# Optimization experiments

Hardware: AMD Instinct MI355X
Metric: run time of the kernel (lower is better)

## Reference

```python
import jax, jax.numpy as jnp
import numpy as np
from jax import lax

N, C, H, W = 16, 1, 512, 512
MAX_ITERS = H + W  # upper bound on flood-fill propagation distance


def _dilate4(r):
    # 3x3 cross (4-connectivity) grayscale dilation, r: (N,H,W)
    rp = jnp.pad(r, ((0, 0), (1, 1), (1, 1)))
    up = rp[:, :-2, 1:-1]
    dn = rp[:, 2:, 1:-1]
    lf = rp[:, 1:-1, :-2]
    rt = rp[:, 1:-1, 2:]
    return jnp.maximum(jnp.maximum(jnp.maximum(up, dn), jnp.maximum(lf, rt)), r)


def _reconstruct_dilation(marker, mask):
    # skimage.morphology.reconstruction(seed, mask, method='dilation'):
    # iterate rec = min(dilate(rec), mask) until convergence.
    def cond(state):
        _, changed, i = state
        return jnp.logical_and(changed, i < MAX_ITERS)

    def body(state):
        r, _, i = state
        nr = jnp.minimum(_dilate4(r), mask)
        return nr, jnp.any(nr != r), i + 1

    rec, _, _ = lax.while_loop(cond, body, (marker, jnp.array(True), jnp.array(0)))
    return rec


def _adaptive_binarize(prob, marker_factor, mask_factor):
    # prob: (N,1,H,W); mirrors torch .detach() -> threshold -> reconstruction
    img = lax.stop_gradient(prob[:, 0])  # (N,H,W)
    nzm = img > 0
    cnt = jnp.sum(nzm, axis=(1, 2))                      # (N,)
    safe = jnp.maximum(cnt, 1).astype(img.dtype)
    mean = jnp.sum(jnp.where(nzm, img, 0.0), axis=(1, 2)) / safe
    var = jnp.sum(jnp.where(nzm, (img - mean[:, None, None]) ** 2, 0.0), axis=(1, 2)) / safe
    std = jnp.sqrt(var)

    def threshold(factor):
        T = (mean + factor * std)[:, None, None]
        b = img > T
        empty = jnp.sum(b, axis=(1, 2)) == 0
        T2 = (mean + (factor / 2.0) * std)[:, None, None]
        b2 = img > T2
        return jnp.where(empty[:, None, None], b2, b)

    marker = threshold(marker_factor).astype(jnp.float32)
    maskb = threshold(mask_factor).astype(jnp.float32)
    rec = _reconstruct_dilation(marker, maskb)
    out = (rec > 0.5).astype(jnp.float32)
    out = jnp.where((cnt == 0)[:, None, None], 0.0, out)  # no nonzero pixels -> zeros
    return out[:, None]  # (N,1,H,W)


def setup_inputs() -> dict:
    key = jax.random.key(0)
    k1, k2 = jax.random.split(key)
    thick_logit = jax.random.normal(k1, (N, C, H, W), dtype=jnp.float32)
    thin_logit = jax.random.normal(k2, (N, C, H, W), dtype=jnp.float32)
    return {"thick_logit": thick_logit, "thin_logit": thin_logit}


def reference(thick_logit, thin_logit):
    thick_prob = jax.nn.sigmoid(thick_logit)
    thin_prob = jax.nn.sigmoid(thin_logit)
    thick_bin = _adaptive_binarize(thick_prob, 2.0, 0.5)
    thin_bin = _adaptive_binarize(thin_prob, 4.0, 0.5)
    fused_bin = jnp.clip(thick_bin + thin_bin, 0.0, 1.0)
    return thick_logit, thin_logit, fused_bin
```

## Files before the change

kernel.cpp:

```cpp
#include <hip/hip_runtime.h>
#include <cstdint>
#include <cstddef>

#define HW 512
#define NPIX (HW * HW)
#define NIMG 16
#define NII 32
#define CHUNKS 64
#define CHUNK_PIX 4096
#define IN_ELEMS (NIMG * NPIX)
#define WORDS_PER_II 4096

#define WS_PARTA   0u
#define WS_STATS   49152u
#define WS_PARTC   50176u
#define WS_SEL     82944u
#define WS_ZMASK   83456u
#define WS_MP      98304u
#define WS_MF      (WS_MP + 1048576u)
#define WS_KP      (WS_MF + 1048576u)
#define WS_KF      (WS_KP + 1048576u)
#define WS_ROUT    (WS_KF + 1048576u)

typedef unsigned long long u64;

__device__ __forceinline__ float sigmoid_f32(float x) {
    return (float)(1.0 / (1.0 + exp(-(double)x)));
}

__global__ void kA_copy_reduce(const float* __restrict__ thick,
                               const float* __restrict__ thin,
                               float* __restrict__ out,
                               double* __restrict__ partA) {
    int b = blockIdx.x;
    int ii = b >> 6;
    int chunk = b & 63;
    int j = ii >> 4, n = ii & 15;
    const float* src = (j == 0 ? thick : thin) + (size_t)n * NPIX;
    float* dst = out + (size_t)j * IN_ELEMS + (size_t)n * NPIX;
    int base = chunk * CHUNK_PIX;

    double s = 0.0, sq = 0.0, c = 0.0;
    for (int i = 0; i < 16; ++i) {
        int e = base + i * 256 + threadIdx.x;
        float x = src[e];
        dst[e] = x;
        float img = sigmoid_f32(x);
        if (img > 0.0f) {
            double d = (double)img;
            s += d; sq += d * d; c += 1.0;
        }
    }
    __shared__ double sm[256], sv[256], sc[256];
    sm[threadIdx.x] = s; sv[threadIdx.x] = sq; sc[threadIdx.x] = c;
    __syncthreads();
    for (int off = 128; off > 0; off >>= 1) {
        if (threadIdx.x < off) {
            sm[threadIdx.x] += sm[threadIdx.x + off];
            sv[threadIdx.x] += sv[threadIdx.x + off];
            sc[threadIdx.x] += sc[threadIdx.x + off];
        }
        __syncthreads();
    }
    if (threadIdx.x == 0) {
        double* p = partA + (size_t)(ii * 64 + chunk) * 3;
        p[0] = sm[0]; p[1] = sv[0]; p[2] = sc[0];
    }
}

__global__ void kB_stats(const double* __restrict__ partA,
                         double* __restrict__ stats) {
    int ii = blockIdx.x;
    int t = threadIdx.x;
    const double* p = partA + (size_t)(ii * 64 + t) * 3;
    double s = p[0], sq = p[1], c = p[2];
    for (int off = 32; off > 0; off >>= 1) {
        s  += __shfl_down(s,  (unsigned)off, 64);
        sq += __shfl_down(sq, (unsigned)off, 64);
        c  += __shfl_down(c,  (unsigned)off, 64);
    }
    if (t == 0) {
        double mean = 0.0, var = 0.0;
        if (c > 0.0) {
            mean = s / c;
            var = sq / c - mean * mean;
            if (var < 0.0) var = 0.0;
        }
        double* o = stats + (size_t)ii * 4;
        o[0] = mean; o[1] = sqrt(var); o[2] = c; o[3] = 0.0;
    }
}

__global__ void kC_bitmaps(const float* __restrict__ thick,
                           const float* __restrict__ thin,
                           const double* __restrict__ stats,
                           u64* __restrict__ mp, u64* __restrict__ mf,
                           u64* __restrict__ kp, u64* __restrict__ kf,
                           long long* __restrict__ partC) {
    int b = blockIdx.x;
    int ii = b >> 6;
    int chunk = b & 63;
    int j = ii >> 4, n = ii & 15;
    const float* src = (j == 0 ? thick : thin) + (size_t)n * NPIX;
    const double* st = stats + (size_t)ii * 4;
    double mean = st[0], sd = st[1];
    double fac = (j == 0) ? 2.0 : 4.0;
    double Tm  = mean + fac * sd;
    double Tmh = mean + (fac * 0.5) * sd;
    double Tk  = mean + 0.5 * sd;
    double Tkh = mean + 0.25 * sd;

    int t = threadIdx.x, lane = t & 63, w = t >> 6;
    long long cM = 0, cK = 0;
    for (int i = 0; i < 16; ++i) {
        int e = chunk * CHUNK_PIX + i * 256 + t;
        float x = src[e];
        double img = (double)sigmoid_f32(x);
        u64 bM  = __ballot(img > Tm);
        u64 bMh = __ballot(img > Tmh);
        u64 bK  = __ballot(img > Tk);
        u64 bKh = __ballot(img > Tkh);
        if (lane == 0) {
            size_t g = (size_t)ii * WORDS_PER_II + (size_t)chunk * 64 + i * 4 + w;
            mp[g] = bM; mf[g] = bMh; kp[g] = bK; kf[g] = bKh;
            cM += (long long)__popcll(bM);
            cK += (long long)__popcll(bK);
        }
    }
    __shared__ long long aM[4], aK[4];
    if (lane == 0) { aM[w] = cM; aK[w] = cK; }
    __syncthreads();
    if (t == 0) {
        long long* p = partC + (size_t)(ii * 64 + chunk) * 2;
        p[0] = aM[0] + aM[1] + aM[2] + aM[3];
        p[1] = aK[0] + aK[1] + aK[2] + aK[3];
    }
}

__global__ void kD_select(const long long* __restrict__ partC,
                          const double* __restrict__ stats,
                          int* __restrict__ sel,
                          u64* __restrict__ zmask) {
    int ii = threadIdx.x;
    if (ii < NII) {
        long long cM = 0, cK = 0;
        for (int c = 0; c < 64; ++c) {
            const long long* p = partC + (size_t)(ii * 64 + c) * 2;
            cM += p[0]; cK += p[1];
        }
        sel[ii * 4 + 0] = (cM == 0) ? 1 : 0;
        sel[ii * 4 + 1] = (cK == 0) ? 1 : 0;
        zmask[ii] = (stats[(size_t)ii * 4 + 2] > 0.0) ? ~0ull : 0ull;
    }
}

__global__ __launch_bounds__(512) void kE_flood(const u64* __restrict__ mp,
                                                const u64* __restrict__ mf,
                                                const u64* __restrict__ kp,
                                                const u64* __restrict__ kf,
                                                const int* __restrict__ sel,
                                                u64* __restrict__ rout) {
    int ii = blockIdx.x;
    const u64* M = (sel[ii * 4 + 0] ? mf : mp) + (size_t)ii * WORDS_PER_II;
    const u64* K = (sel[ii * 4 + 1] ? kf : kp) + (size_t)ii * WORDS_PER_II;

    __shared__ u64 R[WORDS_PER_II];
    __shared__ int changed;
    int t = threadIdx.x;

    u64 kreg[8];
    for (int w = 0; w < 8; ++w) {
        kreg[w] = K[(size_t)t * 8 + w];
        R[w * HW + t] = M[(size_t)t * 8 + w];
    }
    if (t == 0) changed = 0;
    __syncthreads();

    for (int it = 0; it < 1024; ++it) {
        u64 cur[8], up[8], dn[8];
        for (int w = 0; w < 8; ++w) {
            cur[w] = R[w * HW + t];
            up[w] = (t > 0)        ? R[w * HW + (t - 1)] : 0ull;
            dn[w] = (t < HW - 1)   ? R[w * HW + (t + 1)] : 0ull;
        }
        __syncthreads();

        u64 diff = 0;
        for (int w = 0; w < 8; ++w) {
            u64 h = cur[w] | (cur[w] << 1) | (cur[w] >> 1)
                  | (w > 0 ? (cur[w - 1] >> 63) : 0ull)
                  | (w < 7 ? (cur[w + 1] << 63) : 0ull)
                  | up[w] | dn[w];
            u64 nw = h & kreg[w];
            diff |= nw ^ cur[w];
            R[w * HW + t] = nw;
        }
        u64 bal = __ballot(diff != 0ull);
        if ((t & 63) == 0 && bal) atomicOr(&changed, 1);
        __syncthreads();
        int c = changed;
        __syncthreads();
        if (t == 0) changed = 0;
        if (!c) break;
    }

    for (int w = 0; w < 8; ++w)
        rout[(size_t)ii * WORDS_PER_II + (size_t)t * 8 + w] = R[w * HW + t];
}

__global__ void kF_fuse(const u64* __restrict__ rout,
                        const u64* __restrict__ zmask,
                        float* __restrict__ out) {
    size_t gid = (size_t)blockIdx.x * blockDim.x + threadIdx.x;
    size_t p = gid * 4;
    int n = (int)(p >> 18);
    int e = (int)(p & (NPIX - 1));
    size_t gw = (size_t)(e >> 6);
    u64 w = (rout[(size_t)n * WORDS_PER_II + gw] & zmask[n])
          | (rout[(size_t)(16 + n) * WORDS_PER_II + gw] & zmask[16 + n]);
    int sh = e & 63;
    float4 v;
    v.x = ((w >> sh) & 1ull)       ? 1.0f : 0.0f;
    v.y = ((w >> (sh + 1)) & 1ull) ? 1.0f : 0.0f;
    v.z = ((w >> (sh + 2)) & 1ull) ? 1.0f : 0.0f;
    v.w = ((w >> (sh + 3)) & 1ull) ? 1.0f : 0.0f;
    *(float4*)(out + 2 * (size_t)IN_ELEMS + p) = v;
}

extern "C" void kernel_launch(void* const* d_in, const int* in_sizes, int n_in,
                              void* d_out, int out_size, void* d_ws, size_t ws_size,
                              hipStream_t stream) {
    const float* thick = (const float*)d_in[0];
    const float* thin  = (const float*)d_in[1];
    float* out = (float*)d_out;
    char* ws = (char*)d_ws;

    double*    partA = (double*)(ws + WS_PARTA);
    double*    stats = (double*)(ws + WS_STATS);
    long long* partC = (long long*)(ws + WS_PARTC);
    int*       sel   = (int*)(ws + WS_SEL);
    u64*       zmask = (u64*)(ws + WS_ZMASK);
    u64*       mp    = (u64*)(ws + WS_MP);
    u64*       mf    = (u64*)(ws + WS_MF);
    u64*       kp    = (u64*)(ws + WS_KP);
    u64*       kf    = (u64*)(ws + WS_KF);
    u64*       rout  = (u64*)(ws + WS_ROUT);

    kA_copy_reduce<<<NII * CHUNKS, 256, 0, stream>>>(thick, thin, out, partA);
    kB_stats<<<NII, 64, 0, stream>>>(partA, stats);
    kC_bitmaps<<<NII * CHUNKS, 256, 0, stream>>>(thick, thin, stats, mp, mf, kp, kf, partC);
    kD_select<<<1, 64, 0, stream>>>(partC, stats, sel, zmask);
    kE_flood<<<NII, 512, 0, stream>>>(mp, mf, kp, kf, sel, rout);
    kF_fuse<<<4096, 256, 0, stream>>>(rout, zmask, out);
}
```

Before: 157.9 us.

## Rewrite flood fill with register-resident rows and carry-propagation horizontal fill

```diff
diff --git a/kernel.cpp b/kernel.cpp
--- a/kernel.cpp
+++ b/kernel.cpp
@@ -9,46 +9,39 @@
 #define CHUNKS 64
 #define CHUNK_PIX 4096
 #define IN_ELEMS (NIMG * NPIX)
-#define WORDS_PER_II 4096
-
-#define WS_PARTA   0u
-#define WS_STATS   49152u
-#define WS_PARTC   50176u
-#define WS_SEL     82944u
-#define WS_ZMASK   83456u
-#define WS_MP      98304u
-#define WS_MF      (WS_MP + 1048576u)
-#define WS_KP      (WS_MF + 1048576u)
-#define WS_KF      (WS_KP + 1048576u)
-#define WS_ROUT    (WS_KF + 1048576u)
+#define WPI 4096
 
 typedef unsigned long long u64;
+
+#define WS_PARTA 0u
+#define WS_CUT   49152u
+#define WS_ZM    49664u
+#define WS_PARTC 49920u
+#define WS_MP    98304u
+#define WS_MF    (WS_MP + 1048576u)
+#define WS_KP    (WS_MF + 1048576u)
+#define WS_KF    (WS_KP + 1048576u)
+#define WS_ROUT  (WS_KF + 1048576u)
 
 __device__ __forceinline__ float sigmoid_f32(float x) {
     return (float)(1.0 / (1.0 + exp(-(double)x)));
 }
 
-__global__ void kA_copy_reduce(const float* __restrict__ thick,
-                               const float* __restrict__ thin,
-                               float* __restrict__ out,
-                               double* __restrict__ partA) {
+__global__ void k1_stats(const float* __restrict__ A, const float* __restrict__ B,
+                         double* __restrict__ partA) {
     int b = blockIdx.x;
-    int ii = b >> 6;
-    int chunk = b & 63;
-    int j = ii >> 4, n = ii & 15;
-    const float* src = (j == 0 ? thick : thin) + (size_t)n * NPIX;
-    float* dst = out + (size_t)j * IN_ELEMS + (size_t)n * NPIX;
-    int base = chunk * CHUNK_PIX;
-
+    int ii = b >> 6, chunk = b & 63;
+    const float* src = ((ii >> 4) == 0 ? A : B) + (size_t)(ii & 15) * NPIX
+                     + (size_t)chunk * CHUNK_PIX;
     double s = 0.0, sq = 0.0, c = 0.0;
-    for (int i = 0; i < 16; ++i) {
-        int e = base + i * 256 + threadIdx.x;
-        float x = src[e];
-        dst[e] = x;
-        float img = sigmoid_f32(x);
-        if (img > 0.0f) {
-            double d = (double)img;
-            s += d; sq += d * d; c += 1.0;
+#pragma unroll
+    for (int p = 0; p < 4; ++p) {
+        float4 v = *(const float4*)(src + p * 1024 + threadIdx.x * 4);
+        float xs[4] = {v.x, v.y, v.z, v.w};
+#pragma unroll
+        for (int q = 0; q < 4; ++q) {
+            float img = sigmoid_f32(xs[q]);
+            if (img > 0.0f) { double d = (double)img; s += d; sq += d * d; c += 1.0; }
         }
     }
     __shared__ double sm[256], sv[256], sc[256];
@@ -68,10 +61,26 @@
     }
 }
 
-__global__ void kB_stats(const double* __restrict__ partA,
-                         double* __restrict__ stats) {
-    int ii = blockIdx.x;
-    int t = threadIdx.x;
+__device__ __forceinline__ float key_to_f32(unsigned k) {
+    unsigned b = (k & 0x80000000u) ? (k ^ 0x80000000u) : ~k;
+    return __uint_as_float(b);
+}
+__device__ float find_cut(double T) {
+    if (!(1.0 > T)) return __uint_as_float(0x7F800000u);
+    unsigned lo = 0x007FFFFFu;
+    unsigned hi = 0xFF800000u;
+    while (lo < hi) {
+        unsigned mid = lo + ((hi - lo) >> 1);
+        float x = key_to_f32(mid);
+        float s32 = sigmoid_f32(x);
+        if ((double)s32 > T) hi = mid; else lo = mid + 1;
+    }
+    return key_to_f32(lo);
+}
+
+__global__ void kS_cut(const double* __restrict__ partA,
+                       float* __restrict__ cut, u64* __restrict__ zm) {
+    int ii = blockIdx.x, t = threadIdx.x;
     const double* p = partA + (size_t)(ii * 64 + t) * 3;
     double s = p[0], sq = p[1], c = p[2];
     for (int off = 32; off > 0; off >>= 1) {
@@ -79,145 +88,199 @@
         sq += __shfl_down(sq, (unsigned)off, 64);
         c  += __shfl_down(c,  (unsigned)off, 64);
     }
-    if (t == 0) {
-        double mean = 0.0, var = 0.0;
-        if (c > 0.0) {
-            mean = s / c;
-            var = sq / c - mean * mean;
-            if (var < 0.0) var = 0.0;
-        }
-        double* o = stats + (size_t)ii * 4;
-        o[0] = mean; o[1] = sqrt(var); o[2] = c; o[3] = 0.0;
-    }
-}
-
-__global__ void kC_bitmaps(const float* __restrict__ thick,
-                           const float* __restrict__ thin,
-                           const double* __restrict__ stats,
-                           u64* __restrict__ mp, u64* __restrict__ mf,
-                           u64* __restrict__ kp, u64* __restrict__ kf,
-                           long long* __restrict__ partC) {
-    int b = blockIdx.x;
-    int ii = b >> 6;
-    int chunk = b & 63;
+    s = __shfl(s, 0, 64); sq = __shfl(sq, 0, 64); c = __shfl(c, 0, 64);
+    double mean = 0.0, sd = 0.0;
+    if (c > 0.0) {
+        mean = s / c;
+        double var = sq / c - mean * mean;
+        if (var < 0.0) var = 0.0;
+        sd = sqrt(var);
+    }
+    double fac = (ii < 16) ? 2.0 : 4.0;
+    if (t < 4) {
+        double T = (t == 0) ? mean + fac * sd
+                 : (t == 1) ? mean + 0.5 * fac * sd
+                 : (t == 2) ? mean + 0.5 * sd
+                 :            mean + 0.25 * sd;
+        cut[ii * 4 + t] = find_cut(T);
+    }
+    if (t == 0) zm[ii] = (c > 0.0) ? ~0ull : 0ull;
+}
+
+__global__ void k2_bits(const float* __restrict__ A, const float* __restrict__ B,
+                        const float* __restrict__ cut,
+                        u64* __restrict__ mp, u64* __restrict__ mf,
+                        u64* __restrict__ kp, u64* __restrict__ kf,
+                        long long* __restrict__ partC, float* __restrict__ out) {
+    int b = blockIdx.x, ii = b >> 6, chunk = b & 63;
     int j = ii >> 4, n = ii & 15;
-    const float* src = (j == 0 ? thick : thin) + (size_t)n * NPIX;
-    const double* st = stats + (size_t)ii * 4;
-    double mean = st[0], sd = st[1];
-    double fac = (j == 0) ? 2.0 : 4.0;
-    double Tm  = mean + fac * sd;
-    double Tmh = mean + (fac * 0.5) * sd;
-    double Tk  = mean + 0.5 * sd;
-    double Tkh = mean + 0.25 * sd;
+    const float* src = (j == 0 ? A : B) + (size_t)n * NPIX;
+    float* dst = out + (size_t)j * IN_ELEMS + (size_t)n * NPIX;
+    float cM = cut[ii * 4 + 0], cMf = cut[ii * 4 + 1];
+    float cK = cut[ii * 4 + 2], cKf = cut[ii * 4 + 3];
 
     int t = threadIdx.x, lane = t & 63, w = t >> 6;
-    long long cM = 0, cK = 0;
+    long long aM = 0, aK = 0;
+#pragma unroll 4
     for (int i = 0; i < 16; ++i) {
         int e = chunk * CHUNK_PIX + i * 256 + t;
         float x = src[e];
-        double img = (double)sigmoid_f32(x);
-        u64 bM  = __ballot(img > Tm);
-        u64 bMh = __ballot(img > Tmh);
-        u64 bK  = __ballot(img > Tk);
-        u64 bKh = __ballot(img > Tkh);
+        dst[e] = x;
+        u64 bM  = __ballot(x >= cM);
+        u64 bMf = __ballot(x >= cMf);
+        u64 bK  = __ballot(x >= cK);
+        u64 bKf = __ballot(x >= cKf);
         if (lane == 0) {
-            size_t g = (size_t)ii * WORDS_PER_II + (size_t)chunk * 64 + i * 4 + w;
-            mp[g] = bM; mf[g] = bMh; kp[g] = bK; kf[g] = bKh;
-            cM += (long long)__popcll(bM);
-            cK += (long long)__popcll(bK);
-        }
-    }
-    __shared__ long long aM[4], aK[4];
-    if (lane == 0) { aM[w] = cM; aK[w] = cK; }
+            size_t g = (size_t)ii * WPI + (size_t)chunk * 64 + i * 4 + w;
+            mp[g] = bM; mf[g] = bMf; kp[g] = bK; kf[g] = bKf;
+            aM += (long long)__popcll(bM);
+            aK += (long long)__popcll(bK);
+        }
+    }
+    __shared__ long long sM[4], sK[4];
+    if (lane == 0) { sM[w] = aM; sK[w] = aK; }
     __syncthreads();
     if (t == 0) {
         long long* p = partC + (size_t)(ii * 64 + chunk) * 2;
-        p[0] = aM[0] + aM[1] + aM[2] + aM[3];
-        p[1] = aK[0] + aK[1] + aK[2] + aK[3];
-    }
-}
-
-__global__ void kD_select(const long long* __restrict__ partC,
-                          const double* __restrict__ stats,
-                          int* __restrict__ sel,
-                          u64* __restrict__ zmask) {
-    int ii = threadIdx.x;
-    if (ii < NII) {
-        long long cM = 0, cK = 0;
-        for (int c = 0; c < 64; ++c) {
-            const long long* p = partC + (size_t)(ii * 64 + c) * 2;
-            cM += p[0]; cK += p[1];
-        }
-        sel[ii * 4 + 0] = (cM == 0) ? 1 : 0;
-        sel[ii * 4 + 1] = (cK == 0) ? 1 : 0;
-        zmask[ii] = (stats[(size_t)ii * 4 + 2] > 0.0) ? ~0ull : 0ull;
-    }
-}
-
-__global__ __launch_bounds__(512) void kE_flood(const u64* __restrict__ mp,
-                                                const u64* __restrict__ mf,
-                                                const u64* __restrict__ kp,
-                                                const u64* __restrict__ kf,
-                                                const int* __restrict__ sel,
-                                                u64* __restrict__ rout) {
-    int ii = blockIdx.x;
-    const u64* M = (sel[ii * 4 + 0] ? mf : mp) + (size_t)ii * WORDS_PER_II;
-    const u64* K = (sel[ii * 4 + 1] ? kf : kp) + (size_t)ii * WORDS_PER_II;
-
-    __shared__ u64 R[WORDS_PER_II];
-    __shared__ int changed;
-    int t = threadIdx.x;
-
-    u64 kreg[8];
+        p[0] = sM[0] + sM[1] + sM[2] + sM[3];
+        p[1] = sK[0] + sK[1] + sK[2] + sK[3];
+    }
+}
+
+__device__ __forceinline__ void hfill8(u64* x, const u64* k, u64& diff) {
+    u64 f[8];
+    u64 carry = 0;
+#pragma unroll
     for (int w = 0; w < 8; ++w) {
-        kreg[w] = K[(size_t)t * 8 + w];
-        R[w * HW + t] = M[(size_t)t * 8 + w];
-    }
-    if (t == 0) changed = 0;
+        u64 a = k[w], g = x[w];
+        u64 t1 = a + g;  u64 c1 = (u64)(t1 < a);
+        u64 t2 = t1 + carry; u64 c2 = (u64)(t2 < t1);
+        carry = c1 | c2;
+        f[w] = (~t2 | g) & a;
+    }
+    u64 rk[8], rg[8];
+#pragma unroll
+    for (int w = 0; w < 8; ++w) { rk[w] = __brevll(k[7 - w]); rg[w] = __brevll(f[7 - w]); }
+    carry = 0;
+#pragma unroll
+    for (int w = 0; w < 8; ++w) {
+        u64 a = rk[w], g = rg[w];
+        u64 t1 = a + g;  u64 c1 = (u64)(t1 < a);
+        u64 t2 = t1 + carry; u64 c2 = (u64)(t2 < t1);
+        carry = c1 | c2;
+        rg[w] = (~t2 | g) & a;
+    }
+#pragma unroll
+    for (int w = 0; w < 8; ++w) {
+        u64 nx = __brevll(rg[7 - w]);
+        diff |= nx ^ x[w];
+        x[w] = nx;
+    }
+}
+
+__global__ __launch_bounds__(128, 1) void k3_flood(
+        const u64* __restrict__ mp, const u64* __restrict__ mf,
+        const u64* __restrict__ kp, const u64* __restrict__ kf,
+        const long long* __restrict__ partC, u64* __restrict__ rout) {
+    int ii = blockIdx.x, t = threadIdx.x;
+    __shared__ u64 btop[8 * 128], bbot[8 * 128];
+    __shared__ int ssel[2];
+
+    if (t < 64) {
+        long long a = partC[(size_t)(ii * 64 + t) * 2];
+        long long b = partC[(size_t)(ii * 64 + t) * 2 + 1];
+        for (int off = 32; off > 0; off >>= 1) {
+            a += __shfl_down(a, (unsigned)off, 64);
+            b += __shfl_down(b, (unsigned)off, 64);
+        }
+        if (t == 0) { ssel[0] = (a == 0); ssel[1] = (b == 0); }
+    }
     __syncthreads();
-
-    for (int it = 0; it < 1024; ++it) {
-        u64 cur[8], up[8], dn[8];
+    const u64* M = (ssel[0] ? mf : mp) + (size_t)ii * WPI;
+    const u64* K = (ssel[1] ? kf : kp) + (size_t)ii * WPI;
+
+    u64 r[4][8], k[4][8];
+#pragma unroll
+    for (int rr = 0; rr < 4; ++rr)
+#pragma unroll
         for (int w = 0; w < 8; ++w) {
-            cur[w] = R[w * HW + t];
-            up[w] = (t > 0)        ? R[w * HW + (t - 1)] : 0ull;
-            dn[w] = (t < HW - 1)   ? R[w * HW + (t + 1)] : 0ull;
-        }
+            k[rr][w] = K[(size_t)(t * 4 + rr) * 8 + w];
+            r[rr][w] = M[(size_t)(t * 4 + rr) * 8 + w] & k[rr][w];
+        }
+
+#pragma unroll
+    for (int w = 0; w < 8; ++w) { btop[w * 128 + t] = r[0][w]; bbot[w * 128 + t] = r[3][w]; }
+    __syncthreads();
+    u64 nu[8], nd[8];
+#pragma unroll
+    for (int w = 0; w < 8; ++w) {
+        nu[w] = (t > 0)   ? bbot[w * 128 + t - 1] : 0ull;
+        nd[w] = (t < 127) ? btop[w * 128 + t + 1] : 0ull;
+    }
+
+    for (int it = 0; it < 2048; ++it) {
+        u64 diff = 0;
+#pragma unroll
+        for (int w = 0; w < 8; ++w) {
+            u64 a0 = nu[w] & k[0][w] & ~r[0][w]; r[0][w] |= a0; diff |= a0;
+            u64 a3 = nd[w] & k[3][w] & ~r[3][w]; r[3][w] |= a3; diff |= a3;
+        }
+#pragma unroll
+        for (int rr = 1; rr < 4; ++rr)
+#pragma unroll
+            for (int w = 0; w < 8; ++w) {
+                u64 a = r[rr - 1][w] & k[rr][w] & ~r[rr][w]; r[rr][w] |= a; diff |= a;
+            }
+#pragma unroll
+        for (int rr = 2; rr >= 0; --rr)
+#pragma unroll
+            for (int w = 0; w < 8; ++w) {
+                u64 a = r[rr + 1][w] & k[rr][w] & ~r[rr][w]; r[rr][w] |= a; diff |= a;
+            }
+#pragma unroll
+        for (int rr = 0; rr < 4; ++rr) hfill8(r[rr], k[rr], diff);
+#pragma unroll
+        for (int rr = 1; rr < 4; ++rr)
+#pragma unroll
+            for (int w = 0; w < 8; ++w) {
+                u64 a = r[rr - 1][w] & k[rr][w] & ~r[rr][w]; r[rr][w] |= a; diff |= a;
+            }
+#pragma unroll
+        for (int rr = 2; rr >= 0; --rr)
+#pragma unroll
+            for (int w = 0; w < 8; ++w) {
+                u64 a = r[rr + 1][w] & k[rr][w] & ~r[rr][w]; r[rr][w] |= a; diff |= a;
+            }
+#pragma unroll
+        for (int w = 0; w < 8; ++w) { btop[w * 128 + t] = r[0][w]; bbot[w * 128 + t] = r[3][w]; }
         __syncthreads();
-
-        u64 diff = 0;
+        u64 pend = 0;
+#pragma unroll
         for (int w = 0; w < 8; ++w) {
-            u64 h = cur[w] | (cur[w] << 1) | (cur[w] >> 1)
-                  | (w > 0 ? (cur[w - 1] >> 63) : 0ull)
-                  | (w < 7 ? (cur[w + 1] << 63) : 0ull)
-                  | up[w] | dn[w];
-            u64 nw = h & kreg[w];
-            diff |= nw ^ cur[w];
-            R[w * HW + t] = nw;
-        }
-        u64 bal = __ballot(diff != 0ull);
-        if ((t & 63) == 0 && bal) atomicOr(&changed, 1);
-        __syncthreads();
-        int c = changed;
-        __syncthreads();
-        if (t == 0) changed = 0;
-        if (!c) break;
-    }
-
-    for (int w = 0; w < 8; ++w)
-        rout[(size_t)ii * WORDS_PER_II + (size_t)t * 8 + w] = R[w * HW + t];
-}
-
-__global__ void kF_fuse(const u64* __restrict__ rout,
-                        const u64* __restrict__ zmask,
+            nu[w] = (t > 0)   ? bbot[w * 128 + t - 1] : 0ull;
+            nd[w] = (t < 127) ? btop[w * 128 + t + 1] : 0ull;
+            pend |= (nu[w] & k[0][w] & ~r[0][w]) | (nd[w] & k[3][w] & ~r[3][w]);
+        }
+        if (!__syncthreads_or((diff | pend) != 0ull ? 1 : 0)) break;
+    }
+
+#pragma unroll
+    for (int rr = 0; rr < 4; ++rr)
+#pragma unroll
+        for (int w = 0; w < 8; ++w)
+            rout[(size_t)ii * WPI + (size_t)(t * 4 + rr) * 8 + w] = r[rr][w];
+}
+
+__global__ void k4_fuse(const u64* __restrict__ rout,
+                        const u64* __restrict__ zm,
                         float* __restrict__ out) {
     size_t gid = (size_t)blockIdx.x * blockDim.x + threadIdx.x;
     size_t p = gid * 4;
     int n = (int)(p >> 18);
     int e = (int)(p & (NPIX - 1));
     size_t gw = (size_t)(e >> 6);
-    u64 w = (rout[(size_t)n * WORDS_PER_II + gw] & zmask[n])
-          | (rout[(size_t)(16 + n) * WORDS_PER_II + gw] & zmask[16 + n]);
+    u64 w = (rout[(size_t)n * WPI + gw] & zm[n])
+          | (rout[(size_t)(16 + n) * WPI + gw] & zm[16 + n]);
     int sh = e & 63;
     float4 v;
     v.x = ((w >> sh) & 1ull)       ? 1.0f : 0.0f;
@@ -236,20 +299,18 @@
     char* ws = (char*)d_ws;
 
     double*    partA = (double*)(ws + WS_PARTA);
-    double*    stats = (double*)(ws + WS_STATS);
+    float*     cut   = (float*)(ws + WS_CUT);
+    u64*       zm    = (u64*)(ws + WS_ZM);
     long long* partC = (long long*)(ws + WS_PARTC);
-    int*       sel   = (int*)(ws + WS_SEL);
-    u64*       zmask = (u64*)(ws + WS_ZMASK);
     u64*       mp    = (u64*)(ws + WS_MP);
     u64*       mf    = (u64*)(ws + WS_MF);
     u64*       kp    = (u64*)(ws + WS_KP);
     u64*       kf    = (u64*)(ws + WS_KF);
     u64*       rout  = (u64*)(ws + WS_ROUT);
 
-    kA_copy_reduce<<<NII * CHUNKS, 256, 0, stream>>>(thick, thin, out, partA);
-    kB_stats<<<NII, 64, 0, stream>>>(partA, stats);
-    kC_bitmaps<<<NII * CHUNKS, 256, 0, stream>>>(thick, thin, stats, mp, mf, kp, kf, partC);
-    kD_select<<<1, 64, 0, stream>>>(partC, stats, sel, zmask);
-    kE_flood<<<NII, 512, 0, stream>>>(mp, mf, kp, kf, sel, rout);
-    kF_fuse<<<4096, 256, 0, stream>>>(rout, zmask, out);
-}
+    k1_stats<<<NII * CHUNKS, 256, 0, stream>>>(thick, thin, partA);
+    kS_cut<<<NII, 64, 0, stream>>>(partA, cut, zm);
+    k2_bits<<<NII * CHUNKS, 256, 0, stream>>>(thick, thin, cut, mp, mf, kp, kf, partC, out);
+    k3_flood<<<NII, 128, 0, stream>>>(mp, mf, kp, kf, partC, rout);
+    k4_fuse<<<4096, 256, 0, stream>>>(rout, zm, out);
+}
```

After: 368.9 us. 134% more time.
